# Performance work log

Measured on AMD Instinct MI355X. Metric: run time of the kernel, lower is better.

Reference implementation:

```python
import jax, jax.numpy as jnp
import numpy as np

TEMP = 5.0  # temperature_init
# All C(4,2)=6 keep-2-of-4 patterns for 2:4 semi-structured sparsity
PATTERNS = jnp.array([[1,1,0,0],[1,0,1,0],[1,0,0,1],[0,1,1,0],[0,1,0,1],[0,0,1,1]], dtype=jnp.float32)


def masked_linear(x, w, b, alpha, ids):
    # x: [N, I], w: [O, I], alpha: [A, O, I//4, 6], ids: [N]
    A, O, G, P = alpha.shape
    probs = jax.nn.softmax(alpha / TEMP, axis=-1)            # [A, O, G, 6]
    mask = jnp.einsum('aogp,pk->aogk', probs, PATTERNS)      # [A, O, G, 4]
    wm = w[None, :, :] * mask.reshape(A, O, G * 4)           # [A, O, I] per-agent masked weight
    y = jnp.einsum('ni,aoi->nao', x, wm)                     # dense per-agent GEMM
    y = jnp.take_along_axis(y, ids[:, None, None], axis=1)[:, 0, :]
    return y + b


def gru_cell(x, h, w_ih, w_hh, b_ih, b_hh):
    gi = x @ w_ih.T + b_ih
    gh = h @ w_hh.T + b_hh
    i_r, i_z, i_n = jnp.split(gi, 3, axis=-1)
    h_r, h_z, h_n = jnp.split(gh, 3, axis=-1)
    r = jax.nn.sigmoid(i_r + h_r)
    z = jax.nn.sigmoid(i_z + h_z)
    n = jnp.tanh(i_n + r * h_n)
    return (1.0 - z) * n + z * h


def setup_inputs() -> dict:
    key = jax.random.key(0)
    ks = jax.random.split(key, 20)
    B, A, E, H, NA = 1024, 8, 64, 512, 16
    s = 0.05
    d = {}
    d['inputs'] = jax.random.normal(ks[0], (B, A, E), jnp.float32)
    d['hidden_state'] = jax.random.normal(ks[1], (B, A, H), jnp.float32)
    d['agent_ids'] = jax.random.randint(ks[2], (B, A), 0, A, jnp.int32)
    d['fc1_w'] = jax.random.normal(ks[3], (H, E), jnp.float32) * s
    d['fc1_b'] = jax.random.normal(ks[4], (H,), jnp.float32) * s
    d['fc1_alpha'] = jax.random.normal(ks[5], (A, H, E // 4, 6), jnp.float32)
    d['gru_w_ih'] = jax.random.normal(ks[6], (3 * H, H), jnp.float32) * s
    d['gru_w_hh'] = jax.random.normal(ks[7], (3 * H, H), jnp.float32) * s
    d['gru_b_ih'] = jax.random.normal(ks[8], (3 * H,), jnp.float32) * s
    d['gru_b_hh'] = jax.random.normal(ks[9], (3 * H,), jnp.float32) * s
    d['fc2_w'] = jax.random.normal(ks[10], (H, H), jnp.float32) * s
    d['fc2_b'] = jax.random.normal(ks[11], (H,), jnp.float32) * s
    d['fc2_alpha'] = jax.random.normal(ks[12], (A, H, H // 4, 6), jnp.float32)
    d['fc3_w'] = jax.random.normal(ks[13], (H, H), jnp.float32) * s
    d['fc3_b'] = jax.random.normal(ks[14], (H,), jnp.float32) * s
    d['fc3_alpha'] = jax.random.normal(ks[15], (A, H, H // 4, 6), jnp.float32)
    d['fc4_w'] = jax.random.normal(ks[16], (NA, H), jnp.float32) * s
    d['fc4_b'] = jax.random.normal(ks[17], (NA,), jnp.float32) * s
    d['fc4_alpha'] = jax.random.normal(ks[18], (A, NA, H // 4, 6), jnp.float32)
    return d


def reference(inputs, hidden_state, agent_ids,
              fc1_w, fc1_b, fc1_alpha,
              gru_w_ih, gru_w_hh, gru_b_ih, gru_b_hh,
              fc2_w, fc2_b, fc2_alpha,
              fc3_w, fc3_b, fc3_alpha,
              fc4_w, fc4_b, fc4_alpha):
    b, a, e = inputs.shape
    H = hidden_state.shape[-1]
    x = inputs.reshape(-1, e)
    ids = agent_ids.reshape(-1)
    x = jax.nn.relu(masked_linear(x, fc1_w, fc1_b, fc1_alpha, ids))
    h = gru_cell(x, hidden_state.reshape(-1, H), gru_w_ih, gru_w_hh, gru_b_ih, gru_b_hh)
    q = jax.nn.relu(masked_linear(h, fc2_w, fc2_b, fc2_alpha, ids))
    q = jax.nn.relu(masked_linear(q, fc3_w, fc3_b, fc3_alpha, ids))
    q = masked_linear(q, fc4_w, fc4_b, fc4_alpha, ids)
    return q.reshape(b, a, -1), h.reshape(b, a, -1)
```

## Files before the change

### kernel.cpp

```cpp
#include <hip/hip_runtime.h>
#include <hip/hip_bf16.h>

typedef unsigned short ushort_t;
typedef __bf16 bf16x8 __attribute__((ext_vector_type(8)));
typedef unsigned short us8 __attribute__((ext_vector_type(8)));
typedef float f32x4 __attribute__((ext_vector_type(4)));

__device__ __forceinline__ float b2f(ushort_t h) {
    union { unsigned int u; float f; } v; v.u = ((unsigned int)h) << 16; return v.f;
}
__device__ __forceinline__ ushort_t f2b(float f) {
    union { float f; unsigned int u; } v; v.f = f;
    unsigned int u = v.u;
    unsigned int r = (u + 0x7FFFu + ((u >> 16) & 1u)) >> 16;
    return (ushort_t)r;
}
__device__ __forceinline__ float sigmoidf_(float x) {
    return 1.f / (1.f + __expf(-x));
}
__device__ __forceinline__ void store_o(ushort_t* p, float v) { *p = f2b(v); }
__device__ __forceinline__ void store_o(float* p, float v) { *p = v; }

__global__ void fill_kernel(float* out, long long n, float val) {
    long long i = (long long)blockIdx.x * blockDim.x + threadIdx.x;
    if (i < n) out[i] = val;
}

#define PACKSZ(O, K) ((long long)((O) >= 64 ? (O) >> 6 : 1) * ((K) >> 5) * 2048)

__global__ void sort_kernel(const int* __restrict__ ids, int N,
                            int* __restrict__ perm, int* __restrict__ seg,
                            int4* __restrict__ ttab, int* __restrict__ tcount) {
    __shared__ int hist[16][8];
    __shared__ int wbase[16][8];
    __shared__ int atot[8];
    __shared__ int abase[8];
    int tid = threadIdx.x, wave = tid >> 6, lane = tid & 63;
    int base = wave * 512;
    unsigned long long lt = (lane == 63) ? 0x7fffffffffffffffull
                                         : ((1ull << lane) - 1ull);
    int myid[8], rank[8];
    int run[8] = {0, 0, 0, 0, 0, 0, 0, 0};
    #pragma unroll
    for (int i = 0; i < 8; i++) myid[i] = ids[base + i * 64 + lane] & 7;
    #pragma unroll
    for (int i = 0; i < 8; i++) {
        int a = myid[i];
        int r = 0;
        #pragma unroll
        for (int a2 = 0; a2 < 8; a2++) {
            unsigned long long m = __ballot(a == a2);
            if (a2 == a) r = run[a2] + __popcll(m & lt);
            run[a2] += __popcll(m);
        }
        rank[i] = r;
    }
    if (lane == 0) {
        #pragma unroll
        for (int a = 0; a < 8; a++) hist[wave][a] = run[a];
    }
    __syncthreads();
    if (tid < 8) {
        int a = tid, s = 0;
        for (int w = 0; w < 16; w++) { wbase[w][a] = s; s += hist[w][a]; }
        atot[a] = s;
    }
    __syncthreads();
    if (tid == 0) {
        int s = 0;
        for (int a = 0; a < 8; a++) { abase[a] = s; seg[a] = s; s += atot[a]; }
        seg[8] = s;
        int T = 0;
        for (int a = 0; a < 8; a++)
            for (int m = abase[a]; m < abase[a] + atot[a]; m += 64) {
                int e = abase[a] + atot[a];
                if (e > m + 64) e = m + 64;
                ttab[T++] = make_int4(a, m, e, 0);
            }
        *tcount = T;
    }
    __syncthreads();
    #pragma unroll
    for (int i = 0; i < 8; i++) {
        int a = myid[i];
        perm[abase[a] + wbase[wave][a] + rank[i]] = base + i * 64 + lane;
    }
}

__device__ __forceinline__ void maskw_item(const float* __restrict__ alpha,
                                           const float* __restrict__ w,
                                           ushort_t* __restrict__ wm,
                                           long long idx, int O, int G, int dup) {
    int g = (int)(idx % G);
    long long t2 = idx / G;
    int o = (int)(t2 % O);
    int a = (int)(t2 / O);
    const float* al = alpha + idx * 6;
    float p[6];
    float mx = -1e30f;
    #pragma unroll
    for (int i = 0; i < 6; i++) { p[i] = al[i] * 0.2f; mx = fmaxf(mx, p[i]); }
    float s = 0.f;
    #pragma unroll
    for (int i = 0; i < 6; i++) { p[i] = __expf(p[i] - mx); s += p[i]; }
    float inv = 1.f / s;
    #pragma unroll
    for (int i = 0; i < 6; i++) p[i] *= inv;
    float mk[4] = { p[0] + p[1] + p[2], p[0] + p[3] + p[4],
                    p[1] + p[3] + p[5], p[2] + p[4] + p[5] };
    int K = G * 4;
    const float* wr = w + (long long)o * K + g * 4;
    ushort_t* base = wm + (long long)a * PACKSZ(O, K);
    int k0 = g * 4;
    int c = o >> 6, su = (o >> 4) & 3, n = o & 15;
    int kk = k0 >> 5, q = (k0 >> 3) & 3, e0 = k0 & 7;
    long long off = (((long long)(c * (K >> 5) + kk) * 4 + su) * 64 + (q * 16 + n)) * 8 + e0;
    #pragma unroll
    for (int t = 0; t < 4; t++) {
        ushort_t v = f2b(wr[t] * mk[t]);
        base[off + t] = v;
        if (dup) {
            base[off + t + 512] = v;
            base[off + t + 1024] = v;
            base[off + t + 1536] = v;
        }
    }
}

__device__ __forceinline__ void canon_gather_item(const float* __restrict__ src,
                                                  ushort_t* __restrict__ dst,
                                                  const int* __restrict__ perm,
                                                  int ld, long long i) {
    long long base = i * 8;
    int pos = (int)(base / ld);
    int k = (int)(base % ld);
    int row = perm[pos] & 8191;
    const float* s = src + (long long)row * ld + k;
    us8 v;
    #pragma unroll
    for (int e = 0; e < 8; e++) v[e] = f2b(s[e]);
    *(us8*)(dst + base) = v;
}

__device__ __forceinline__ void canon_pack_item(const float* __restrict__ src,
                                                ushort_t* __restrict__ dst,
                                                long long i) {
    long long base = i * 8;
    int o_full = (int)(base >> 9);
    int k0 = (int)(base & 511);
    int g = o_full >> 9, o = o_full & 511;
    int c = o >> 6, su = (o >> 4) & 3, n = o & 15;
    int kk = k0 >> 5, q = (k0 >> 3) & 3;
    long long off = (long long)g * 262144 +
        (((long long)(c * 16 + kk) * 4 + su) * 64 + (q * 16 + n)) * 8;
    us8 v;
    #pragma unroll
    for (int e = 0; e < 8; e++) v[e] = f2b(src[base + e]);
    *(us8*)(dst + off) = v;
}

#define PB0 256
#define PB1 2048
#define PB2 2048
#define PB3 64
#define PB4 256
#define PB5 2048
#define PB6 384
#define PB7 384
#define PREP_BLOCKS (PB0+PB1+PB2+PB3+PB4+PB5+PB6+PB7)

__global__ void prep_kernel(const float* fc1_al, const float* fc1_w, ushort_t* wm1,
                            const float* fc2_al, const float* fc2_w, ushort_t* wm2,
                            const float* fc3_al, const float* fc3_w, ushort_t* wm3,
                            const float* fc4_al, const float* fc4_w, ushort_t* wm4,
                            const float* inputs, ushort_t* inp_pos,
                            const float* hidden, ushort_t* hid_pos,
                            const float* wih, ushort_t* wihp,
                            const float* whh, ushort_t* whhp,
                            const int* perm) {
    int b = blockIdx.x;
    int tid = threadIdx.x;
    if (b < PB0) { maskw_item(fc1_al, fc1_w, wm1, (long long)b * 256 + tid, 512, 16, 0); return; }
    b -= PB0;
    if (b < PB1) { maskw_item(fc2_al, fc2_w, wm2, (long long)b * 256 + tid, 512, 128, 0); return; }
    b -= PB1;
    if (b < PB2) { maskw_item(fc3_al, fc3_w, wm3, (long long)b * 256 + tid, 512, 128, 0); return; }
    b -= PB2;
    if (b < PB3) { maskw_item(fc4_al, fc4_w, wm4, (long long)b * 256 + tid, 16, 128, 1); return; }
    b -= PB3;
    if (b < PB4) { canon_gather_item(inputs, inp_pos, perm, 64, (long long)b * 256 + tid); return; }
    b -= PB4;
    if (b < PB5) { canon_gather_item(hidden, hid_pos, perm, 512, (long long)b * 256 + tid); return; }
    b -= PB5;
    if (b < PB6) { canon_pack_item(wih, wihp, (long long)b * 256 + tid); return; }
    b -= PB6;
    canon_pack_item(whh, whhp, (long long)b * 256 + tid);
}

#define BM 64
#define BN 64

template <typename OT>
__launch_bounds__(256, 4)
__global__ void gemm_tiled(const ushort_t* __restrict__ In, int ldin,
                           const ushort_t* __restrict__ Wpk, long long wstride,
                           const float* __restrict__ bias,
                           OT* __restrict__ Out, int ldo,
                           const int4* __restrict__ ttab,
                           const int* __restrict__ tcount,
                           const int* __restrict__ scatter,
                           int O, int K, int relu) {
    int t = blockIdx.x;
    if (t >= *tcount) return;
    int4 tt = ttab[t];
    int a = tt.x, pos0 = tt.y, pos1 = tt.z;
    int o0 = blockIdx.y * BN;

    __shared__ ushort_t As[2048];

    int tid = threadIdx.x;
    int wave = tid >> 6, lane = tid & 63;
    int wr = (wave >> 1) & 1, wc = wave & 1;
    int quad = lane >> 4, l16 = lane & 15;
    int srow = tid >> 2, sgrp = tid & 3;
    int wsoff = (srow * 4 + (sgrp ^ ((srow >> 2) & 3))) * 8;
    int rl = (l16 * 4 + (quad ^ ((l16 >> 2) & 3))) * 8;

    int apos = pos0 + srow;
    int apos_c = apos < pos1 ? apos : (pos1 - 1);
    const ushort_t* aptr = In + (long long)apos_c * ldin + sgrp * 8;

    const ushort_t* wb = Wpk + (long long)a * wstride +
        (long long)blockIdx.y * (K >> 5) * 2048 + lane * 8;

    f32x4 acc[2][2];
    #pragma unroll
    for (int i = 0; i < 2; i++)
        #pragma unroll
        for (int j = 0; j < 2; j++) acc[i][j] = (f32x4){0.f, 0.f, 0.f, 0.f};

    int KK = K >> 5;
    for (int kk = 0; kk < KK; kk++) {
        us8 av = *(const us8*)(aptr + kk * 32);
        bf16x8 bfr[2];
        bfr[0] = *(const bf16x8*)(wb + (kk * 4 + wc * 2 + 0) * 512);
        bfr[1] = *(const bf16x8*)(wb + (kk * 4 + wc * 2 + 1) * 512);
        __syncthreads();
        *(us8*)(&As[wsoff]) = av;
        __syncthreads();
        bf16x8 af[2];
        af[0] = *(const bf16x8*)(&As[(wr * 2 + 0) * 512 + rl]);
        af[1] = *(const bf16x8*)(&As[(wr * 2 + 1) * 512 + rl]);
        #pragma unroll
        for (int i = 0; i < 2; i++)
            #pragma unroll
            for (int j = 0; j < 2; j++)
                acc[i][j] = __builtin_amdgcn_mfma_f32_16x16x32_bf16(af[i], bfr[j], acc[i][j], 0, 0, 0);
    }

    #pragma unroll
    for (int i = 0; i < 2; i++) {
        int mbase = wr * 32 + i * 16 + quad * 4;
        #pragma unroll
        for (int j = 0; j < 2; j++) {
            int col = o0 + wc * 32 + j * 16 + l16;
            if (col < O) {
                float bias_v = bias ? bias[col] : 0.f;
                #pragma unroll
                for (int r = 0; r < 4; r++) {
                    int pos = pos0 + mbase + r;
                    if (pos < pos1) {
                        float v = acc[i][j][r] + bias_v;
                        if (relu) v = fmaxf(v, 0.f);
                        int orow = (scatter ? scatter[pos] : pos) & 8191;
                        store_o(&Out[(long long)orow * ldo + col], v);
                    }
                }
            }
        }
    }
}

__launch_bounds__(256, 3)
__global__ void gru_fused(const ushort_t* __restrict__ y1,
                          const ushort_t* __restrict__ hid_pos,
                          const float* __restrict__ hidden_f,
                          const ushort_t* __restrict__ wihp,
                          const ushort_t* __restrict__ whhp,
                          const float* __restrict__ bih,
                          const float* __restrict__ bhh,
                          const int* __restrict__ perm,
                          float* __restrict__ out_h_f,
                          ushort_t* __restrict__ hp,
                          int N, int H) {
    int m0 = blockIdx.x * 64;

    __shared__ ushort_t Ay[2048];
    __shared__ ushort_t Ah[2048];
    __shared__ ushort_t Bt[6][2048];

    int tid = threadIdx.x;
    int wave = tid >> 6, lane = tid & 63;
    int wr = (wave >> 1) & 1, wc = wave & 1;
    int quad = lane >> 4, l16 = lane & 15;
    int srow = tid >> 2, sgrp = tid & 3;
    int wsoff = (srow * 4 + (sgrp ^ ((srow >> 2) & 3))) * 8;
    int rl = (l16 * 4 + (quad ^ ((l16 >> 2) & 3))) * 8;

    const ushort_t* ay_p = y1 + (long long)(m0 + srow) * H + sgrp * 8;
    const ushort_t* ah_p = hid_pos + (long long)(m0 + srow) * H + sgrp * 8;

    long long cb = (long long)blockIdx.y * 16 * 2048 + tid * 8;
    const ushort_t* wbg[6];
    #pragma unroll
    for (int g = 0; g < 3; g++) wbg[g] = wihp + (long long)g * 262144 + cb;
    #pragma unroll
    for (int g = 3; g < 6; g++) wbg[g] = whhp + (long long)(g - 3) * 262144 + cb;

    f32x4 acc[4][2][2];
    #pragma unroll
    for (int g = 0; g < 4; g++)
        #pragma unroll
        for (int i = 0; i < 2; i++)
            #pragma unroll
            for (int j = 0; j < 2; j++) acc[g][i][j] = (f32x4){0.f, 0.f, 0.f, 0.f};

    for (int kk = 0; kk < 16; kk++) {
        us8 va = *(const us8*)(ay_p + kk * 32);
        us8 vh = *(const us8*)(ah_p + kk * 32);
        us8 vb[6];
        #pragma unroll
        for (int g = 0; g < 6; g++) vb[g] = *(const us8*)(wbg[g] + kk * 2048);
        __syncthreads();
        *(us8*)(&Ay[wsoff]) = va;
        *(us8*)(&Ah[wsoff]) = vh;
        #pragma unroll
        for (int g = 0; g < 6; g++) *(us8*)(&Bt[g][tid * 8]) = vb[g];
        __syncthreads();

        bf16x8 ayf[2], ahf[2];
        #pragma unroll
        for (int u = 0; u < 2; u++) {
            ayf[u] = *(const bf16x8*)(&Ay[(wr * 2 + u) * 512 + rl]);
            ahf[u] = *(const bf16x8*)(&Ah[(wr * 2 + u) * 512 + rl]);
        }
        #pragma unroll
        for (int g = 0; g < 3; g++) {
            bf16x8 bw[2], bu[2];
            #pragma unroll
            for (int u = 0; u < 2; u++) {
                bw[u] = *(const bf16x8*)(&Bt[g][(wc * 2 + u) * 512 + lane * 8]);
                bu[u] = *(const bf16x8*)(&Bt[g + 3][(wc * 2 + u) * 512 + lane * 8]);
            }
            int ai = (g < 2) ? g : 2;
            int ah2 = (g < 2) ? g : 3;
            #pragma unroll
            for (int i = 0; i < 2; i++)
                #pragma unroll
                for (int j = 0; j < 2; j++) {
                    acc[ai][i][j] = __builtin_amdgcn_mfma_f32_16x16x32_bf16(
                        ayf[i], bw[j], acc[ai][i][j], 0, 0, 0);
                    acc[ah2][i][j] = __builtin_amdgcn_mfma_f32_16x16x32_bf16(
                        ahf[i], bu[j], acc[ah2][i][j], 0, 0, 0);
                }
        }
    }

    int c0 = blockIdx.y * 64;
    #pragma unroll
    for (int i = 0; i < 2; i++) {
        #pragma unroll
        for (int r = 0; r < 4; r++) {
            int pos = m0 + wr * 32 + i * 16 + quad * 4 + r;
            int norig = perm[pos] & 8191;
            #pragma unroll
            for (int j = 0; j < 2; j++) {
                int col = c0 + wc * 32 + j * 16 + l16;
                float sr = acc[0][i][j][r] + bih[col] + bhh[col];
                float sz = acc[1][i][j][r] + bih[H + col] + bhh[H + col];
                float in_ = acc[2][i][j][r] + bih[2 * H + col];
                float hn = acc[3][i][j][r] + bhh[2 * H + col];
                float rg = sigmoidf_(sr);
                float zg = sigmoidf_(sz);
                float ng = tanhf(in_ + rg * hn);
                float hv = hidden_f[(long long)norig * H + col];
                float hnew = (1.f - zg) * ng + zg * hv;
                out_h_f[(long long)norig * H + col] = hnew;
                hp[(long long)pos * H + col] = f2b(hnew);
            }
        }
    }
}

extern "C" void kernel_launch(void* const* d_in, const int* in_sizes, int n_in,
                              void* d_out, int out_size, void* d_ws, size_t ws_size,
                              hipStream_t stream) {
    (void)in_sizes; (void)n_in;
    const int N = 8192, A = 8, E = 64, H = 512, NA = 16;

    float* out_f = (float*)d_out;
    float* out_q = out_f;
    float* out_h = out_f + (size_t)N * NA;

    char* p = (char*)d_ws;
    auto alloc = [&](size_t b) { char* r = p; p += (b + 255) & ~(size_t)255; return r; };
    int*  perm   = (int*)alloc((size_t)N * 4);
    int*  seg    = (int*)alloc(16 * 4);
    int4* ttab   = (int4*)alloc(144 * 16);
    int*  tcount = (int*)alloc(256);
    ushort_t* wm1     = (ushort_t*)alloc((size_t)A * PACKSZ(H, E) * 2);
    ushort_t* wm2     = (ushort_t*)alloc((size_t)A * PACKSZ(H, H) * 2);
    ushort_t* wm3     = (ushort_t*)alloc((size_t)A * PACKSZ(H, H) * 2);
    ushort_t* wm4     = (ushort_t*)alloc((size_t)A * PACKSZ(NA, H) * 2);
    ushort_t* y1      = (ushort_t*)alloc((size_t)N * H * 2);
    ushort_t* inp_pos = (ushort_t*)alloc((size_t)N * E * 2);
    ushort_t* hid_pos = (ushort_t*)alloc((size_t)N * H * 2);
    ushort_t* wihp    = (ushort_t*)alloc((size_t)3 * H * H * 2);
    ushort_t* whhp    = (ushort_t*)alloc((size_t)3 * H * H * 2);
    ushort_t* hp      = (ushort_t*)alloc((size_t)N * H * 2);
    size_t need = (size_t)(p - (char*)d_ws);
    ushort_t* q2 = y1;
    ushort_t* q3 = hid_pos;

    if (ws_size < need) {
        fill_kernel<<<(unsigned)((out_size + 255) / 256), 256, 0, stream>>>(
            out_f, out_size, 1000.f);
        return;
    }

    const float* inputs = (const float*)d_in[0];
    const float* hidden = (const float*)d_in[1];
    const int*   ids    = (const int*)d_in[2];
    const float* fc1_w  = (const float*)d_in[3];
    const float* fc1_b  = (const float*)d_in[4];
    const float* fc1_al = (const float*)d_in[5];
    const float* wih    = (const float*)d_in[6];
    const float* whh    = (const float*)d_in[7];
    const float* bih    = (const float*)d_in[8];
    const float* bhh    = (const float*)d_in[9];
    const float* fc2_w  = (const float*)d_in[10];
    const float* fc2_b  = (const float*)d_in[11];
    const float* fc2_al = (const float*)d_in[12];
    const float* fc3_w  = (const float*)d_in[13];
    const float* fc3_b  = (const float*)d_in[14];
    const float* fc3_al = (const float*)d_in[15];
    const float* fc4_w  = (const float*)d_in[16];
    const float* fc4_b  = (const float*)d_in[17];
    const float* fc4_al = (const float*)d_in[18];

    sort_kernel<<<1, 1024, 0, stream>>>(ids, N, perm, seg, ttab, tcount);

    prep_kernel<<<PREP_BLOCKS, 256, 0, stream>>>(
        fc1_al, fc1_w, wm1, fc2_al, fc2_w, wm2, fc3_al, fc3_w, wm3,
        fc4_al, fc4_w, wm4, inputs, inp_pos, hidden, hid_pos,
        wih, wihp, whh, whhp, perm);

    dim3 blk(256);
    gemm_tiled<ushort_t><<<dim3(136, H / BN), blk, 0, stream>>>(
        inp_pos, E, wm1, PACKSZ(H, E), fc1_b, y1, H, ttab, tcount,
        nullptr, H, E, 1);
    gru_fused<<<dim3(N / 64, H / 64), blk, 0, stream>>>(
        y1, hid_pos, hidden, wihp, whhp, bih, bhh, perm, out_h, hp, N, H);
    gemm_tiled<ushort_t><<<dim3(136, H / BN), blk, 0, stream>>>(
        hp, H, wm2, PACKSZ(H, H), fc2_b, q2, H, ttab, tcount,
        nullptr, H, H, 1);
    gemm_tiled<ushort_t><<<dim3(136, H / BN), blk, 0, stream>>>(
        q2, H, wm3, PACKSZ(H, H), fc3_b, q3, H, ttab, tcount,
        nullptr, H, H, 1);
    gemm_tiled<float><<<dim3(136, 1), blk, 0, stream>>>(
        q3, H, wm4, PACKSZ(NA, H), fc4_b, out_q, NA, ttab, tcount,
        perm, NA, H, 0);
}
```

Before: 227.5 us.

## Prefetch next K tile into registers and stage weights via LDS in GEMMs

Both the tiled GEMM and the fused GRU kernel now issue the global loads for iteration k+1 right after the LDS barrier, before the MFMA work of iteration k, so memory latency overlaps with compute. The tiled GEMM also changes how it reads weights: each thread loads one distinct 8-element chunk and stages it in a new shared buffer, instead of each wave reading its B fragments straight from global memory, which removes duplicate global reads across waves. Launch-bound occupancy hints are raised from 4 to 6 and from 3 to 4. The prefetch keeps more values live in registers, and the higher occupancy targets may force register spills.

```diff
diff --git a/kernel.cpp b/kernel.cpp
--- a/kernel.cpp
+++ b/kernel.cpp
@@ -201,7 +201,7 @@
 #define BN 64
 
 template <typename OT>
-__launch_bounds__(256, 4)
+__launch_bounds__(256, 6)
 __global__ void gemm_tiled(const ushort_t* __restrict__ In, int ldin,
                            const ushort_t* __restrict__ Wpk, long long wstride,
                            const float* __restrict__ bias,
@@ -217,6 +217,7 @@
     int o0 = blockIdx.y * BN;
 
     __shared__ ushort_t As[2048];
+    __shared__ ushort_t Bs[2048];
 
     int tid = threadIdx.x;
     int wave = tid >> 6, lane = tid & 63;
@@ -229,9 +230,8 @@
     int apos = pos0 + srow;
     int apos_c = apos < pos1 ? apos : (pos1 - 1);
     const ushort_t* aptr = In + (long long)apos_c * ldin + sgrp * 8;
-
-    const ushort_t* wb = Wpk + (long long)a * wstride +
-        (long long)blockIdx.y * (K >> 5) * 2048 + lane * 8;
+    const ushort_t* bptr = Wpk + (long long)a * wstride +
+        (long long)blockIdx.y * (K >> 5) * 2048 + tid * 8;
 
     f32x4 acc[2][2];
     #pragma unroll
@@ -240,17 +240,23 @@
         for (int j = 0; j < 2; j++) acc[i][j] = (f32x4){0.f, 0.f, 0.f, 0.f};
 
     int KK = K >> 5;
+    us8 av = *(const us8*)(aptr);
+    us8 bv = *(const us8*)(bptr);
     for (int kk = 0; kk < KK; kk++) {
-        us8 av = *(const us8*)(aptr + kk * 32);
-        bf16x8 bfr[2];
-        bfr[0] = *(const bf16x8*)(wb + (kk * 4 + wc * 2 + 0) * 512);
-        bfr[1] = *(const bf16x8*)(wb + (kk * 4 + wc * 2 + 1) * 512);
         __syncthreads();
         *(us8*)(&As[wsoff]) = av;
+        *(us8*)(&Bs[tid * 8]) = bv;
         __syncthreads();
-        bf16x8 af[2];
-        af[0] = *(const bf16x8*)(&As[(wr * 2 + 0) * 512 + rl]);
-        af[1] = *(const bf16x8*)(&As[(wr * 2 + 1) * 512 + rl]);
+        int kn = (kk + 1 < KK) ? kk + 1 : kk;
+        av = *(const us8*)(aptr + kn * 32);
+        bv = *(const us8*)(bptr + kn * 2048);
+
+        bf16x8 af[2], bfr[2];
+        #pragma unroll
+        for (int u = 0; u < 2; u++) {
+            af[u]  = *(const bf16x8*)(&As[(wr * 2 + u) * 512 + rl]);
+            bfr[u] = *(const bf16x8*)(&Bs[(wc * 2 + u) * 512 + lane * 8]);
+        }
         #pragma unroll
         for (int i = 0; i < 2; i++)
             #pragma unroll
@@ -281,7 +287,7 @@
     }
 }
 
-__launch_bounds__(256, 3)
+__launch_bounds__(256, 4)
 __global__ void gru_fused(const ushort_t* __restrict__ y1,
                           const ushort_t* __restrict__ hid_pos,
                           const float* __restrict__ hidden_f,
@@ -325,18 +331,25 @@
             #pragma unroll
             for (int j = 0; j < 2; j++) acc[g][i][j] = (f32x4){0.f, 0.f, 0.f, 0.f};
 
+    us8 va = *(const us8*)(ay_p);
+    us8 vh = *(const us8*)(ah_p);
+    us8 vb[6];
+    #pragma unroll
+    for (int g = 0; g < 6; g++) vb[g] = *(const us8*)(wbg[g]);
+
     for (int kk = 0; kk < 16; kk++) {
-        us8 va = *(const us8*)(ay_p + kk * 32);
-        us8 vh = *(const us8*)(ah_p + kk * 32);
-        us8 vb[6];
-        #pragma unroll
-        for (int g = 0; g < 6; g++) vb[g] = *(const us8*)(wbg[g] + kk * 2048);
         __syncthreads();
         *(us8*)(&Ay[wsoff]) = va;
         *(us8*)(&Ah[wsoff]) = vh;
         #pragma unroll
         for (int g = 0; g < 6; g++) *(us8*)(&Bt[g][tid * 8]) = vb[g];
         __syncthreads();
+
+        int kn = (kk + 1 < 16) ? kk + 1 : kk;
+        va = *(const us8*)(ay_p + kn * 32);
+        vh = *(const us8*)(ah_p + kn * 32);
+        #pragma unroll
+        for (int g = 0; g < 6; g++) vb[g] = *(const us8*)(wbg[g] + kn * 2048);
 
         bf16x8 ayf[2], ahf[2];
         #pragma unroll
```

New measurement: 233.8 us. 1.03x slower.
